# Optimization experiments

Hardware: AMD Instinct MI355X
Metric: run time of the kernel (lower is better)

Reference implementation:

```python
import jax, jax.numpy as jnp
import numpy as np

K, N = 64, 4096

def setup_inputs() -> dict:
    key = jax.random.key(0)
    k1, k2 = jax.random.split(key)
    zs = jax.random.uniform(k1, (K, N), dtype=jnp.float32)        # K candidate schedules
    X = jax.random.uniform(k2, (N, N), dtype=jnp.float32)         # channel gain matrix
    var_noise = jnp.asarray(1.0, dtype=jnp.float32)
    return {"zs": zs, "X": X, "var_noise": var_noise}

def reference(zs, X, var_noise):
    # Original per-sample math: all_info[i,j] = z[j]*X[i,j]
    #   numerators   = diag(all_info) = z * diag(X)
    #   denominators = row_sum(all_info) - numerators = X @ z - numerators
    # Batched over K zs: one GEMM instead of K O(n^2) elementwise products.
    row_sums = jnp.einsum('kn,in->ki', zs, X)       # [K, N] = (X @ z_k)_i
    numerators = zs * jnp.diagonal(X)[None, :]      # [K, N]
    denominators = row_sums - numerators            # [K, N]
    per_sample = -jnp.sum(numerators / (var_noise + denominators), axis=1)  # [K]
    return jnp.sum(per_sample) / zs.shape[0]
```

## Files before the change

kernel.cpp:

```cpp
#include <hip/hip_runtime.h>

#define N_DIM 4096

typedef float f4  __attribute__((ext_vector_type(4)));
typedef short s8v __attribute__((ext_vector_type(8)));

static __device__ __forceinline__ unsigned short f2bf(float f) {
    unsigned int u = __builtin_bit_cast(unsigned int, f);
    u = (u + 0x7fffu + ((u >> 16) & 1u)) >> 16;
    return (unsigned short)u;
}
static __device__ __forceinline__ s8v pack8(f4 a, f4 b) {
    s8v h;
    h[0] = (short)f2bf(a[0]); h[1] = (short)f2bf(a[1]);
    h[2] = (short)f2bf(a[2]); h[3] = (short)f2bf(a[3]);
    h[4] = (short)f2bf(b[0]); h[5] = (short)f2bf(b[1]);
    h[6] = (short)f2bf(b[2]); h[7] = (short)f2bf(b[3]);
    return h;
}

__global__ void zero_out_kernel(float* __restrict__ out) {
    if (threadIdx.x == 0 && blockIdx.x == 0) out[0] = 0.f;
}

__global__ __launch_bounds__(256, 1) void fused_kernel(
    const float* __restrict__ zs, const float* __restrict__ X,
    const float* __restrict__ varp, float* __restrict__ out) {
    __shared__ s8v zs_l[2][1024];
    __shared__ s8v x_l [2][256];

    const int tid  = threadIdx.x;
    const int lane = tid & 63;
    const int w    = tid >> 6;
    const int i0   = blockIdx.x * 16;

    f4 acc = {0.f, 0.f, 0.f, 0.f};
    f4 rz[8], rx[2];

    #pragma unroll
    for (int it = 0; it < 4; ++it) {
        int idx = it * 256 + tid;
        const f4* g = (const f4*)(zs + ((idx >> 8) * 16 + (idx & 15)) * N_DIM
                                     + ((idx >> 4) & 15) * 8);
        rz[2 * it] = g[0]; rz[2 * it + 1] = g[1];
    }
    {
        const f4* gx = (const f4*)(X + (size_t)(i0 + (tid & 15)) * N_DIM
                                      + ((tid >> 4) & 15) * 8);
        rx[0] = gx[0]; rx[1] = gx[1];
    }
    #pragma unroll
    for (int it = 0; it < 4; ++it)
        zs_l[0][it * 256 + tid] = pack8(rz[2 * it], rz[2 * it + 1]);
    x_l[0][tid] = pack8(rx[0], rx[1]);

    for (int c = 0; c < 32; ++c) {
        const int cur = c & 1, nxt = cur ^ 1;
        if (c < 31) {
            const int n0 = (c + 1) * 128;
            #pragma unroll
            for (int it = 0; it < 4; ++it) {
                int idx = it * 256 + tid;
                const f4* g = (const f4*)(zs + ((idx >> 8) * 16 + (idx & 15)) * N_DIM
                                             + n0 + ((idx >> 4) & 15) * 8);
                rz[2 * it] = g[0]; rz[2 * it + 1] = g[1];
            }
            const f4* gx = (const f4*)(X + (size_t)(i0 + (tid & 15)) * N_DIM
                                          + n0 + ((tid >> 4) & 15) * 8);
            rx[0] = gx[0]; rx[1] = gx[1];
        }
        __syncthreads();
        #pragma unroll
        for (int s = 0; s < 4; ++s) {
            s8v a = zs_l[cur][(w * 4 + s) * 64 + lane];
            s8v b = x_l[cur][s * 64 + lane];
            acc = __builtin_amdgcn_mfma_f32_16x16x32_bf16(a, b, acc, 0, 0, 0);
        }
        if (c < 31) {
            #pragma unroll
            for (int it = 0; it < 4; ++it)
                zs_l[nxt][it * 256 + tid] = pack8(rz[2 * it], rz[2 * it + 1]);
            x_l[nxt][tid] = pack8(rx[0], rx[1]);
        }
    }

    const int   i_g  = i0 + (lane & 15);
    const float diag = X[(size_t)i_g * N_DIM + i_g];
    const float var  = varp[0];
    float lsum = 0.f;
    #pragma unroll
    for (int r = 0; r < 4; ++r) {
        int   k   = 16 * w + ((lane >> 4) << 2) + r;
        float num = zs[k * N_DIM + i_g] * diag;
        float den = acc[r] - num;
        lsum += num / (var + den);
    }
    #pragma unroll
    for (int off = 32; off >= 1; off >>= 1) lsum += __shfl_down(lsum, off);
    __shared__ float wsum[4];
    if (lane == 0) wsum[w] = lsum;
    __syncthreads();
    if (tid == 0)
        atomicAdd(out, -(wsum[0] + wsum[1] + wsum[2] + wsum[3]) * (1.0f / 64.0f));
}

extern "C" void kernel_launch(void* const* d_in, const int* in_sizes, int n_in,
                              void* d_out, int out_size, void* d_ws, size_t ws_size,
                              hipStream_t stream) {
    const float* zs   = (const float*)d_in[0];
    const float* X    = (const float*)d_in[1];
    const float* varp = (const float*)d_in[2];
    float* out = (float*)d_out;

    hipLaunchKernelGGL(zero_out_kernel, dim3(1), dim3(64), 0, stream, out);
    hipLaunchKernelGGL(fused_kernel, dim3(256), dim3(256), 0, stream, zs, X, varp, out);
}
```

Measured before the change: 130.3 us.

## Load MFMA operands directly from global into registers, dropping LDS staging

Removes the shared-memory double buffer and per-chunk __syncthreads. Each wave now loads its zs and X fragments straight from global memory into registers, prefetching the next chunk while the current one runs on MFMA. Float-to-bf16 conversion uses the packed cvt builtin when it is available, and launch_bounds no longer forces one block per CU. The cost is that the X tile is now reloaded by all four waves instead of being shared through LDS, which raises global and L2 traffic.

```diff
diff --git a/kernel.cpp b/kernel.cpp
--- a/kernel.cpp
+++ b/kernel.cpp
@@ -5,83 +5,83 @@
 typedef float f4  __attribute__((ext_vector_type(4)));
 typedef short s8v __attribute__((ext_vector_type(8)));
 
-static __device__ __forceinline__ unsigned short f2bf(float f) {
-    unsigned int u = __builtin_bit_cast(unsigned int, f);
-    u = (u + 0x7fffu + ((u >> 16) & 1u)) >> 16;
-    return (unsigned short)u;
+#if defined(__has_builtin)
+#if __has_builtin(__builtin_amdgcn_cvt_pk_bf16_f32)
+#define HAVE_CVT_PK 1
+#endif
+#endif
+
+static __device__ __forceinline__ unsigned int f2bf_pair(float lo, float hi) {
+#ifdef HAVE_CVT_PK
+    typedef __bf16 bf2 __attribute__((ext_vector_type(2)));
+    bf2 p = __builtin_amdgcn_cvt_pk_bf16_f32(lo, hi);
+    return __builtin_bit_cast(unsigned int, p);
+#else
+    unsigned int ul = __builtin_bit_cast(unsigned int, lo);
+    unsigned int uh = __builtin_bit_cast(unsigned int, hi);
+    ul = ul + 0x7fffu + ((ul >> 16) & 1u);
+    uh = uh + 0x7fffu + ((uh >> 16) & 1u);
+    return (uh & 0xffff0000u) | (ul >> 16);
+#endif
 }
-static __device__ __forceinline__ s8v pack8(f4 a, f4 b) {
-    s8v h;
-    h[0] = (short)f2bf(a[0]); h[1] = (short)f2bf(a[1]);
-    h[2] = (short)f2bf(a[2]); h[3] = (short)f2bf(a[3]);
-    h[4] = (short)f2bf(b[0]); h[5] = (short)f2bf(b[1]);
-    h[6] = (short)f2bf(b[2]); h[7] = (short)f2bf(b[3]);
-    return h;
+
+static __device__ __forceinline__ s8v cvt8(f4 a, f4 b) {
+    unsigned int r0 = f2bf_pair(a[0], a[1]);
+    unsigned int r1 = f2bf_pair(a[2], a[3]);
+    unsigned int r2 = f2bf_pair(b[0], b[1]);
+    unsigned int r3 = f2bf_pair(b[2], b[3]);
+    unsigned int u4[4] = {r0, r1, r2, r3};
+    return __builtin_bit_cast(s8v, u4);
 }
 
 __global__ void zero_out_kernel(float* __restrict__ out) {
     if (threadIdx.x == 0 && blockIdx.x == 0) out[0] = 0.f;
 }
 
-__global__ __launch_bounds__(256, 1) void fused_kernel(
+__global__ __launch_bounds__(256) void fused_kernel(
     const float* __restrict__ zs, const float* __restrict__ X,
     const float* __restrict__ varp, float* __restrict__ out) {
-    __shared__ s8v zs_l[2][1024];
-    __shared__ s8v x_l [2][256];
-
     const int tid  = threadIdx.x;
     const int lane = tid & 63;
     const int w    = tid >> 6;
     const int i0   = blockIdx.x * 16;
+    const int coff = (lane >> 4) * 8;
+
+    const float* pz = zs + (size_t)(16 * w + (lane & 15)) * N_DIM + coff;
+    const float* px = X  + (size_t)(i0   + (lane & 15)) * N_DIM + coff;
 
     f4 acc = {0.f, 0.f, 0.f, 0.f};
-    f4 rz[8], rx[2];
+    f4 za[8], xb[8];
 
     #pragma unroll
-    for (int it = 0; it < 4; ++it) {
-        int idx = it * 256 + tid;
-        const f4* g = (const f4*)(zs + ((idx >> 8) * 16 + (idx & 15)) * N_DIM
-                                     + ((idx >> 4) & 15) * 8);
-        rz[2 * it] = g[0]; rz[2 * it + 1] = g[1];
+    for (int s = 0; s < 4; ++s) {
+        za[2 * s]     = *(const f4*)(pz + s * 32);
+        za[2 * s + 1] = *(const f4*)(pz + s * 32 + 4);
+        xb[2 * s]     = *(const f4*)(px + s * 32);
+        xb[2 * s + 1] = *(const f4*)(px + s * 32 + 4);
     }
-    {
-        const f4* gx = (const f4*)(X + (size_t)(i0 + (tid & 15)) * N_DIM
-                                      + ((tid >> 4) & 15) * 8);
-        rx[0] = gx[0]; rx[1] = gx[1];
-    }
-    #pragma unroll
-    for (int it = 0; it < 4; ++it)
-        zs_l[0][it * 256 + tid] = pack8(rz[2 * it], rz[2 * it + 1]);
-    x_l[0][tid] = pack8(rx[0], rx[1]);
 
     for (int c = 0; c < 32; ++c) {
-        const int cur = c & 1, nxt = cur ^ 1;
-        if (c < 31) {
-            const int n0 = (c + 1) * 128;
-            #pragma unroll
-            for (int it = 0; it < 4; ++it) {
-                int idx = it * 256 + tid;
-                const f4* g = (const f4*)(zs + ((idx >> 8) * 16 + (idx & 15)) * N_DIM
-                                             + n0 + ((idx >> 4) & 15) * 8);
-                rz[2 * it] = g[0]; rz[2 * it + 1] = g[1];
-            }
-            const f4* gx = (const f4*)(X + (size_t)(i0 + (tid & 15)) * N_DIM
-                                          + n0 + ((tid >> 4) & 15) * 8);
-            rx[0] = gx[0]; rx[1] = gx[1];
-        }
-        __syncthreads();
+        s8v af[4], bf[4];
         #pragma unroll
         for (int s = 0; s < 4; ++s) {
-            s8v a = zs_l[cur][(w * 4 + s) * 64 + lane];
-            s8v b = x_l[cur][s * 64 + lane];
-            acc = __builtin_amdgcn_mfma_f32_16x16x32_bf16(a, b, acc, 0, 0, 0);
+            af[s] = cvt8(za[2 * s], za[2 * s + 1]);
+            bf[s] = cvt8(xb[2 * s], xb[2 * s + 1]);
         }
         if (c < 31) {
+            const float* qz = pz + (c + 1) * 128;
+            const float* qx = px + (c + 1) * 128;
             #pragma unroll
-            for (int it = 0; it < 4; ++it)
-                zs_l[nxt][it * 256 + tid] = pack8(rz[2 * it], rz[2 * it + 1]);
-            x_l[nxt][tid] = pack8(rx[0], rx[1]);
+            for (int s = 0; s < 4; ++s) {
+                za[2 * s]     = *(const f4*)(qz + s * 32);
+                za[2 * s + 1] = *(const f4*)(qz + s * 32 + 4);
+                xb[2 * s]     = *(const f4*)(qx + s * 32);
+                xb[2 * s + 1] = *(const f4*)(qx + s * 32 + 4);
+            }
         }
+        #pragma unroll
+        for (int s = 0; s < 4; ++s)
+            acc = __builtin_amdgcn_mfma_f32_16x16x32_bf16(af[s], bf[s], acc, 0, 0, 0);
     }
 
     const int   i_g  = i0 + (lane & 15);
@@ -91,7 +91,7 @@
     #pragma unroll
     for (int r = 0; r < 4; ++r) {
         int   k   = 16 * w + ((lane >> 4) << 2) + r;
-        float num = zs[k * N_DIM + i_g] * diag;
+        float num = zs[(size_t)k * N_DIM + i_g] * diag;
         float den = acc[r] - num;
         lsum += num / (var + den);
     }
```

Measured after the change: 145.7 us. 11.8% more time.
